# Kernel optimization log

Hardware: AMD Instinct MI355X
Metric: run time of the kernel (lower is better)

The kernel has to match this reference:

```python
import jax, jax.numpy as jnp
import numpy as np

HEADS = 16
DIM_HEAD = 64


def setup_inputs() -> dict:
    key = jax.random.key(0)
    k1, k2, k3 = jax.random.split(key, 3)
    b, n, dim = 4, 2048, 1024
    inner = HEADS * DIM_HEAD  # 1024
    x = jax.random.normal(k1, (b, n, dim), dtype=jnp.float32)
    # Dense weights, scaled like Glorot-ish init to keep softmax well-behaved
    w_qkv = jax.random.normal(k2, (dim, 3 * inner), dtype=jnp.float32) * (dim ** -0.5)
    w_out = jax.random.normal(k3, (inner, dim), dtype=jnp.float32) * (inner ** -0.5)
    b_out = jnp.zeros((dim,), dtype=jnp.float32)
    return {"x": x, "w_qkv": w_qkv, "w_out": w_out, "b_out": b_out}


def reference(x, w_qkv, w_out, b_out):
    b, n, dim = x.shape
    scale = DIM_HEAD ** -0.5
    qkv = x @ w_qkv  # [b, n, 3*h*d]
    q, k, v = jnp.split(qkv, 3, axis=-1)
    # 'b n (h d) -> b h n d'
    split_heads = lambda t: t.reshape(b, n, HEADS, DIM_HEAD).transpose(0, 2, 1, 3)
    q, k, v = split_heads(q), split_heads(k), split_heads(v)
    sim = jnp.einsum('bhid,bhjd->bhij', q, k) * scale  # [b, h, n, n]
    attn = jax.nn.softmax(sim, axis=-1)
    out = jnp.einsum('bhij,bhjd->bhid', attn, v)  # [b, h, n, d]
    out = out.transpose(0, 2, 1, 3).reshape(b, n, HEADS * DIM_HEAD)
    return out @ w_out + b_out  # dropout rate 0.0 -> identity
```

## Files before the change

### kernel.cpp

```cpp
#include <hip/hip_runtime.h>
#include <cstdint>

#define HEADS 16
#define DH 64
#define SEQ 2048
#define BATCH 4
#define DIM 1024
#define MTOT (BATCH*SEQ)
#define NQKV (3*DIM)

typedef short bf16x8 __attribute__((ext_vector_type(8)));
typedef float f32x4 __attribute__((ext_vector_type(4)));
typedef float f32x16 __attribute__((ext_vector_type(16)));

__device__ __forceinline__ unsigned short f2bf(float f) {
  union { float fv; unsigned int u; } c; c.fv = f;
  unsigned int u = c.u;
  u += 0x7FFFu + ((u >> 16) & 1u);
  return (unsigned short)(u >> 16);
}

__device__ __forceinline__ unsigned int pkbf(float lo, float hi) {
  union { float fv; unsigned int u; } a, b; a.fv = lo; b.fv = hi;
  return ((a.u + 0x8000u) >> 16) | ((b.u + 0x8000u) & 0xFFFF0000u);
}

__device__ __forceinline__ f32x4 mfma16(bf16x8 a, bf16x8 b, f32x4 c) {
  return __builtin_amdgcn_mfma_f32_16x16x32_bf16(a, b, c, 0, 0, 0);
}
__device__ __forceinline__ f32x16 mfma32(bf16x8 a, bf16x8 b, f32x16 c) {
  return __builtin_amdgcn_mfma_f32_32x32x16_bf16(a, b, c, 0, 0, 0);
}

typedef const __attribute__((address_space(1))) unsigned int* gas_ptr;
typedef __attribute__((address_space(3))) unsigned int* las_ptr;
__device__ __forceinline__ void gl2lds16(const void* g, void* l) {
  __builtin_amdgcn_global_load_lds((gas_ptr)g, (las_ptr)l, 16, 0, 0);
}

#define QSCALE 0.18033688011112042f

__global__ __launch_bounds__(256) void cast_f32_bf16(
    const float* __restrict__ in, unsigned short* __restrict__ out, int n4) {
  int i = blockIdx.x * blockDim.x + threadIdx.x;
  if (i >= n4) return;
  float4 v = reinterpret_cast<const float4*>(in)[i];
  uint2 o;
  o.x = (unsigned int)f2bf(v.x) | ((unsigned int)f2bf(v.y) << 16);
  o.y = (unsigned int)f2bf(v.z) | ((unsigned int)f2bf(v.w) << 16);
  reinterpret_cast<uint2*>(out)[i] = o;
}

__global__ __launch_bounds__(256) void transpose_cast(
    const float* __restrict__ in, unsigned short* __restrict__ out, int R, int C) {
  __shared__ float tile[32][33];
  int c0 = blockIdx.x * 32, r0 = blockIdx.y * 32;
  int tx = threadIdx.x & 31, ty = threadIdx.x >> 5;
  for (int i = 0; i < 32; i += 8)
    tile[ty + i][tx] = in[(size_t)(r0 + ty + i) * C + c0 + tx];
  __syncthreads();
  for (int i = 0; i < 32; i += 8)
    out[(size_t)(c0 + ty + i) * R + r0 + tx] = f2bf(tile[tx][ty + i]);
}

__global__ __launch_bounds__(256) void transpose_v(
    const unsigned short* __restrict__ V, unsigned short* __restrict__ Vt) {
  __shared__ unsigned short tile[64][72];
  int n0 = blockIdx.x * 64;
  size_t base = (size_t)blockIdx.y * SEQ * DH;
  int t = threadIdx.x;
  int r = t >> 2, c = (t & 3) * 8;
  *(uint4*)&tile[r][c]      = *(const uint4*)&V[base + (size_t)(n0 + r) * DH + c];
  *(uint4*)&tile[r][c + 32] = *(const uint4*)&V[base + (size_t)(n0 + r) * DH + c + 32];
  __syncthreads();
#pragma unroll
  for (int p = 0; p < 2; p++) {
    alignas(16) unsigned short tmp[8];
#pragma unroll
    for (int i = 0; i < 8; i++) tmp[i] = tile[c + p * 32 + i][r];
    *(uint4*)&Vt[base + (size_t)r * SEQ + n0 + c + p * 32] = *(uint4*)tmp;
  }
}

#define BM 128
#define BN 128
#define BK 32
#define LDT 32

__global__ __launch_bounds__(256) void gemm_qkv(
    const unsigned short* __restrict__ A, const unsigned short* __restrict__ Bt,
    unsigned short* __restrict__ Q, unsigned short* __restrict__ K,
    unsigned short* __restrict__ V) {
  __shared__ unsigned short sA[BM * LDT];
  __shared__ unsigned short sB[BN * LDT];
  const int KD = 1024;
  int m0 = blockIdx.y * BM;
  int n0 = blockIdx.x * BN;
  int t = threadIdx.x;
  int lane = t & 63, w = t >> 6;
  int wm = (w >> 1) * 64, wn = (w & 1) * 64;
  int fr = lane & 15, fq = (lane >> 4) * 8;

  const unsigned short* gA = &A[(size_t)(m0 + w * 16 + (lane >> 2)) * KD + (lane & 3) * 8];
  const unsigned short* gB = &Bt[(size_t)(n0 + w * 16 + (lane >> 2)) * KD + (lane & 3) * 8];
  char* lA = (char*)sA + w * 1024;
  char* lB = (char*)sB + w * 1024;

  f32x4 acc[4][4];
#pragma unroll
  for (int i = 0; i < 4; i++)
#pragma unroll
    for (int j = 0; j < 4; j++) { f32x4 z = {0.f, 0.f, 0.f, 0.f}; acc[i][j] = z; }

  for (int k0 = 0; k0 < KD; k0 += BK) {
    gl2lds16(gA + k0, lA);
    gl2lds16(gA + (size_t)64 * KD + k0, lA + 4096);
    gl2lds16(gB + k0, lB);
    gl2lds16(gB + (size_t)64 * KD + k0, lB + 4096);
    __syncthreads();
    bf16x8 af[4], bfr[4];
#pragma unroll
    for (int mt = 0; mt < 4; mt++)
      af[mt] = *reinterpret_cast<const bf16x8*>(&sA[(wm + mt * 16 + fr) * LDT + fq]);
#pragma unroll
    for (int nt = 0; nt < 4; nt++)
      bfr[nt] = *reinterpret_cast<const bf16x8*>(&sB[(wn + nt * 16 + fr) * LDT + fq]);
#pragma unroll
    for (int mt = 0; mt < 4; mt++)
#pragma unroll
      for (int nt = 0; nt < 4; nt++)
        acc[mt][nt] = mfma16(af[mt], bfr[nt], acc[mt][nt]);
    __syncthreads();
  }
  int rowq = (lane >> 4) * 4;
#pragma unroll
  for (int mt = 0; mt < 4; mt++)
#pragma unroll
    for (int nt = 0; nt < 4; nt++)
#pragma unroll
      for (int r = 0; r < 4; r++) {
        int m = m0 + wm + mt * 16 + rowq + r;
        int ncol = n0 + wn + nt * 16 + fr;
        int which = ncol >> 10;
        int hd = ncol & 1023;
        int b = m >> 11, nrow = m & 2047;
        float v = acc[mt][nt][r];
        if (which == 0) v *= QSCALE;
        unsigned short* dst = (which == 0) ? Q : (which == 1 ? K : V);
        size_t idx = ((size_t)(b * HEADS + (hd >> 6)) * SEQ + nrow) * DH + (hd & 63);
        dst[idx] = f2bf(v);
      }
}

__global__ __launch_bounds__(256) void gemm_out(
    const unsigned short* __restrict__ A, const unsigned short* __restrict__ Bt,
    const float* __restrict__ bias, float* __restrict__ C) {
  __shared__ unsigned short sA[BM * LDT];
  __shared__ unsigned short sB[BN * LDT];
  const int KD = 1024;
  int m0 = blockIdx.y * BM;
  int n0 = blockIdx.x * BN;
  int t = threadIdx.x;
  int lane = t & 63, w = t >> 6;
  int wm = (w >> 1) * 64, wn = (w & 1) * 64;
  int fr = lane & 15, fq = (lane >> 4) * 8;

  const unsigned short* gA = &A[(size_t)(m0 + w * 16 + (lane >> 2)) * KD + (lane & 3) * 8];
  const unsigned short* gB = &Bt[(size_t)(n0 + w * 16 + (lane >> 2)) * KD + (lane & 3) * 8];
  char* lA = (char*)sA + w * 1024;
  char* lB = (char*)sB + w * 1024;

  f32x4 acc[4][4];
#pragma unroll
  for (int i = 0; i < 4; i++)
#pragma unroll
    for (int j = 0; j < 4; j++) { f32x4 z = {0.f, 0.f, 0.f, 0.f}; acc[i][j] = z; }

  for (int k0 = 0; k0 < KD; k0 += BK) {
    gl2lds16(gA + k0, lA);
    gl2lds16(gA + (size_t)64 * KD + k0, lA + 4096);
    gl2lds16(gB + k0, lB);
    gl2lds16(gB + (size_t)64 * KD + k0, lB + 4096);
    __syncthreads();
    bf16x8 af[4], bfr[4];
#pragma unroll
    for (int mt = 0; mt < 4; mt++)
      af[mt] = *reinterpret_cast<const bf16x8*>(&sA[(wm + mt * 16 + fr) * LDT + fq]);
#pragma unroll
    for (int nt = 0; nt < 4; nt++)
      bfr[nt] = *reinterpret_cast<const bf16x8*>(&sB[(wn + nt * 16 + fr) * LDT + fq]);
#pragma unroll
    for (int mt = 0; mt < 4; mt++)
#pragma unroll
      for (int nt = 0; nt < 4; nt++)
        acc[mt][nt] = mfma16(af[mt], bfr[nt], acc[mt][nt]);
    __syncthreads();
  }
  int rowq = (lane >> 4) * 4;
#pragma unroll
  for (int mt = 0; mt < 4; mt++)
#pragma unroll
    for (int nt = 0; nt < 4; nt++)
#pragma unroll
      for (int r = 0; r < 4; r++) {
        int m = m0 + wm + mt * 16 + rowq + r;
        int ncol = n0 + wn + nt * 16 + fr;
        C[(size_t)m * DIM + ncol] = acc[mt][nt][r] + bias[ncol];
      }
}

#define LDA 72

__global__ __launch_bounds__(256, 2) void attention(
    const unsigned short* __restrict__ Qg, const unsigned short* __restrict__ Kg,
    const unsigned short* __restrict__ Vtg, unsigned short* __restrict__ Og) {
  __shared__ unsigned short smem[2 * 64 * LDA];
  unsigned short* sK  = smem;
  unsigned short* sVt = smem + 64 * LDA;
  int qb = blockIdx.x, h = blockIdx.y, b = blockIdx.z;
  size_t base = (size_t)(b * HEADS + h) * SEQ * DH;
  const unsigned short* Q = Qg + base;
  const unsigned short* K = Kg + base;
  const unsigned short* Vt = Vtg + base;
  int t = threadIdx.x, lane = t & 63, w = t >> 6;
  int m = lane & 31, kh = lane >> 5;
  int q0 = qb * 256 + w * 64;

  bf16x8 qf[2][4];
#pragma unroll
  for (int qh = 0; qh < 2; qh++)
#pragma unroll
    for (int kt = 0; kt < 4; kt++)
      qf[qh][kt] = *reinterpret_cast<const bf16x8*>(
          &Q[(size_t)(q0 + 32 * qh + m) * DH + kt * 16 + kh * 8]);

  f32x16 oaccT[2][2];
#pragma unroll
  for (int qh = 0; qh < 2; qh++)
#pragma unroll
    for (int dh = 0; dh < 2; dh++)
#pragma unroll
      for (int i = 0; i < 16; i++) oaccT[qh][dh][i] = 0.f;
  float rs[2] = {0.f, 0.f};

  int sr = t >> 2, sc = (t & 3) * 8;

  for (int j0 = 0; j0 < SEQ; j0 += 64) {
    *(uint4*)&sK[sr * LDA + sc]       = *(const uint4*)&K[(size_t)(j0 + sr) * DH + sc];
    *(uint4*)&sK[sr * LDA + sc + 32]  = *(const uint4*)&K[(size_t)(j0 + sr) * DH + sc + 32];
    *(uint4*)&sVt[sr * LDA + sc]      = *(const uint4*)&Vt[(size_t)sr * SEQ + j0 + sc];
    *(uint4*)&sVt[sr * LDA + sc + 32] = *(const uint4*)&Vt[(size_t)sr * SEQ + j0 + sc + 32];
    __syncthreads();

    unsigned int pp[2][8][2];
#pragma unroll
    for (int jt = 0; jt < 2; jt++) {
      bf16x8 kf[4];
#pragma unroll
      for (int kt = 0; kt < 4; kt++)
        kf[kt] = *reinterpret_cast<const bf16x8*>(
            &sK[(jt * 32 + m) * LDA + (2 * kt + kh) * 8]);
#pragma unroll
      for (int qh = 0; qh < 2; qh++) {
        f32x16 s;
#pragma unroll
        for (int i = 0; i < 16; i++) s[i] = 0.f;
#pragma unroll
        for (int kt = 0; kt < 4; kt++)
          s = mfma32(kf[kt], qf[qh][kt], s);
        float e[16];
#pragma unroll
        for (int i = 0; i < 16; i++) e[i] = __builtin_amdgcn_exp2f(s[i]);
        float t0 = (e[0] + e[1]) + (e[2] + e[3]);
        float t1 = (e[4] + e[5]) + (e[6] + e[7]);
        float t2 = (e[8] + e[9]) + (e[10] + e[11]);
        float t3 = (e[12] + e[13]) + (e[14] + e[15]);
        rs[qh] += (t0 + t1) + (t2 + t3);
#pragma unroll
        for (int sl = 0; sl < 4; sl++) {
          pp[qh][4 * jt + sl][0] = pkbf(e[4 * sl + 0], e[4 * sl + 1]);
          pp[qh][4 * jt + sl][1] = pkbf(e[4 * sl + 2], e[4 * sl + 3]);
        }
      }
    }

#pragma unroll
    for (int kb = 0; kb < 4; kb++) {
#pragma unroll
      for (int dh = 0; dh < 2; dh++) {
        union { uint2 u[2]; bf16x8 v; } ac;
        ac.u[0] = *(const uint2*)&sVt[(32 * dh + m) * LDA + 16 * kb + 4 * kh];
        ac.u[1] = *(const uint2*)&sVt[(32 * dh + m) * LDA + 16 * kb + 8 + 4 * kh];
#pragma unroll
        for (int qh = 0; qh < 2; qh++) {
          union { unsigned int u[4]; bf16x8 v; } bc;
          bc.u[0] = pp[qh][2 * kb][0];
          bc.u[1] = pp[qh][2 * kb][1];
          bc.u[2] = pp[qh][2 * kb + 1][0];
          bc.u[3] = pp[qh][2 * kb + 1][1];
          oaccT[qh][dh] = mfma32(ac.v, bc.v, oaccT[qh][dh]);
        }
      }
    }
    __syncthreads();
  }

  float inv[2];
#pragma unroll
  for (int qh = 0; qh < 2; qh++) {
    float tot = rs[qh] + __shfl_xor(rs[qh], 32);
    inv[qh] = 1.0f / tot;
  }

  unsigned int* ew = (unsigned int*)smem + (size_t)w * 32 * 36;
#pragma unroll
  for (int qh = 0; qh < 2; qh++) {
#pragma unroll
    for (int dh = 0; dh < 2; dh++)
#pragma unroll
      for (int sl = 0; sl < 4; sl++) {
        unsigned int u0 = pkbf(oaccT[qh][dh][4 * sl + 0] * inv[qh],
                               oaccT[qh][dh][4 * sl + 1] * inv[qh]);
        unsigned int u1 = pkbf(oaccT[qh][dh][4 * sl + 2] * inv[qh],
                               oaccT[qh][dh][4 * sl + 3] * inv[qh]);
        uint2 pk; pk.x = u0; pk.y = u1;
        *(uint2*)&ew[m * 36 + 16 * dh + 4 * sl + 2 * kh] = pk;
      }
    int mr = lane >> 3, ch = lane & 7;
#pragma unroll
    for (int it = 0; it < 4; it++) {
      uint4 vv = *(const uint4*)&ew[(8 * it + mr) * 36 + ch * 4];
      int n = q0 + 32 * qh + 8 * it + mr;
      *(uint4*)&Og[((size_t)(b * SEQ + n)) * DIM + h * DH + ch * 8] = vv;
    }
  }
}

extern "C" void kernel_launch(void* const* d_in, const int* in_sizes, int n_in,
                              void* d_out, int out_size, void* d_ws, size_t ws_size,
                              hipStream_t stream) {
  const float* x     = (const float*)d_in[0];
  const float* w_qkv = (const float*)d_in[1];
  const float* w_out = (const float*)d_in[2];
  const float* b_out = (const float*)d_in[3];
  float* out = (float*)d_out;

  char* ws = (char*)d_ws;
  unsigned short* xb     = (unsigned short*)ws; ws += (size_t)MTOT * DIM * 2;
  unsigned short* wqkv_t = (unsigned short*)ws; ws += (size_t)NQKV * DIM * 2;
  unsigned short* wout_t = (unsigned short*)ws; ws += (size_t)DIM * DIM * 2;
  unsigned short* qb_    = (unsigned short*)ws; ws += (size_t)BATCH * HEADS * SEQ * DH * 2;
  unsigned short* kb_    = (unsigned short*)ws; ws += (size_t)BATCH * HEADS * SEQ * DH * 2;
  unsigned short* vb_    = (unsigned short*)ws; ws += (size_t)BATCH * HEADS * SEQ * DH * 2;
  unsigned short* attnb  = (unsigned short*)ws; ws += (size_t)MTOT * DIM * 2;
  unsigned short* vt_    = xb;

  cast_f32_bf16<<<(MTOT * DIM / 4 + 255) / 256, 256, 0, stream>>>(x, xb, MTOT * DIM / 4);
  transpose_cast<<<dim3(NQKV / 32, DIM / 32), 256, 0, stream>>>(w_qkv, wqkv_t, DIM, NQKV);
  transpose_cast<<<dim3(DIM / 32, DIM / 32), 256, 0, stream>>>(w_out, wout_t, DIM, DIM);

  gemm_qkv<<<dim3(NQKV / BN, MTOT / BM), 256, 0, stream>>>(xb, wqkv_t, qb_, kb_, vb_);

  transpose_v<<<dim3(SEQ / 64, BATCH * HEADS), 256, 0, stream>>>(vb_, vt_);

  attention<<<dim3(SEQ / 256, HEADS, BATCH), 256, 0, stream>>>(qb_, kb_, vt_, attnb);

  gemm_out<<<dim3(DIM / BN, MTOT / BM), 256, 0, stream>>>(attnb, wout_t, b_out, out);
}
```

Before: 273.6 us.

## Shrink attention query tile, raise occupancy, swizzle block order, use hardware bf16 pack

Each attention block now covers 128 query rows instead of 256, so each wave owns 32 rows instead of 64. The kernel is launched with twice as many blocks and a launch bound of 4 blocks per CU, cutting register pressure so more waves can hide latency. Block indices are remapped so that consecutive blocks spread over different (batch, head) pairs, and the LDS row stride is changed from 72 to 68 with 8-byte stores and loads. Float-to-bf16 packing now uses the v_cvt_pk_bf16_f32 instruction in place of integer bit manipulation. In exchange, K/V tiles are loaded twice as often per query row, which doubles global and LDS traffic per unit of compute.

After: 269.5 us. About the same (-1.5%).

```diff
diff --git a/kernel.cpp b/kernel.cpp
--- a/kernel.cpp
+++ b/kernel.cpp
@@ -20,9 +20,10 @@
   return (unsigned short)(u >> 16);
 }
 
-__device__ __forceinline__ unsigned int pkbf(float lo, float hi) {
-  union { float fv; unsigned int u; } a, b; a.fv = lo; b.fv = hi;
-  return ((a.u + 0x8000u) >> 16) | ((b.u + 0x8000u) & 0xFFFF0000u);
+__device__ __forceinline__ unsigned int cvtpk(float lo, float hi) {
+  unsigned int r;
+  asm("v_cvt_pk_bf16_f32 %0, %1, %2" : "=v"(r) : "v"(lo), "v"(hi));
+  return r;
 }
 
 __device__ __forceinline__ f32x4 mfma16(bf16x8 a, bf16x8 b, f32x4 c) {
@@ -209,78 +210,94 @@
       }
 }
 
-#define LDA 72
-
-__global__ __launch_bounds__(256, 2) void attention(
+#define LDA 68
+
+__global__ __launch_bounds__(256, 4) void attention(
     const unsigned short* __restrict__ Qg, const unsigned short* __restrict__ Kg,
     const unsigned short* __restrict__ Vtg, unsigned short* __restrict__ Og) {
-  __shared__ unsigned short smem[2 * 64 * LDA];
+  __shared__ unsigned short smem[2 * 64 * 72];
   unsigned short* sK  = smem;
   unsigned short* sVt = smem + 64 * LDA;
-  int qb = blockIdx.x, h = blockIdx.y, b = blockIdx.z;
+
+  int gid = blockIdx.x + 16 * (blockIdx.y + 16 * blockIdx.z);
+  int qb   = (gid >> 3) & 15;
+  int pair = ((gid & 7) << 3) | (gid >> 7);
+  int h = pair & 15, b = pair >> 4;
+
   size_t base = (size_t)(b * HEADS + h) * SEQ * DH;
   const unsigned short* Q = Qg + base;
   const unsigned short* K = Kg + base;
   const unsigned short* Vt = Vtg + base;
   int t = threadIdx.x, lane = t & 63, w = t >> 6;
   int m = lane & 31, kh = lane >> 5;
-  int q0 = qb * 256 + w * 64;
-
-  bf16x8 qf[2][4];
-#pragma unroll
-  for (int qh = 0; qh < 2; qh++)
-#pragma unroll
-    for (int kt = 0; kt < 4; kt++)
-      qf[qh][kt] = *reinterpret_cast<const bf16x8*>(
-          &Q[(size_t)(q0 + 32 * qh + m) * DH + kt * 16 + kh * 8]);
-
-  f32x16 oaccT[2][2];
-#pragma unroll
-  for (int qh = 0; qh < 2; qh++)
-#pragma unroll
-    for (int dh = 0; dh < 2; dh++)
-#pragma unroll
-      for (int i = 0; i < 16; i++) oaccT[qh][dh][i] = 0.f;
-  float rs[2] = {0.f, 0.f};
+  int q0 = qb * 128 + w * 32;
+
+  bf16x8 qf[4];
+#pragma unroll
+  for (int kt = 0; kt < 4; kt++)
+    qf[kt] = *reinterpret_cast<const bf16x8*>(
+        &Q[(size_t)(q0 + m) * DH + kt * 16 + kh * 8]);
+
+  f32x16 oaccT[2];
+#pragma unroll
+  for (int dh = 0; dh < 2; dh++)
+#pragma unroll
+    for (int i = 0; i < 16; i++) oaccT[dh][i] = 0.f;
+  float rs = 0.f;
 
   int sr = t >> 2, sc = (t & 3) * 8;
 
   for (int j0 = 0; j0 < SEQ; j0 += 64) {
-    *(uint4*)&sK[sr * LDA + sc]       = *(const uint4*)&K[(size_t)(j0 + sr) * DH + sc];
-    *(uint4*)&sK[sr * LDA + sc + 32]  = *(const uint4*)&K[(size_t)(j0 + sr) * DH + sc + 32];
-    *(uint4*)&sVt[sr * LDA + sc]      = *(const uint4*)&Vt[(size_t)sr * SEQ + j0 + sc];
-    *(uint4*)&sVt[sr * LDA + sc + 32] = *(const uint4*)&Vt[(size_t)sr * SEQ + j0 + sc + 32];
-    __syncthreads();
-
-    unsigned int pp[2][8][2];
+    {
+      uint4 a0 = *(const uint4*)&K[(size_t)(j0 + sr) * DH + sc];
+      uint4 a1 = *(const uint4*)&K[(size_t)(j0 + sr) * DH + sc + 32];
+      uint4 b0 = *(const uint4*)&Vt[(size_t)sr * SEQ + j0 + sc];
+      uint4 b1 = *(const uint4*)&Vt[(size_t)sr * SEQ + j0 + sc + 32];
+      unsigned short* pk0 = &sK[sr * LDA + sc];
+      unsigned short* pk1 = &sK[sr * LDA + sc + 32];
+      unsigned short* pv0 = &sVt[sr * LDA + sc];
+      unsigned short* pv1 = &sVt[sr * LDA + sc + 32];
+      *(uint2*)pk0       = make_uint2(a0.x, a0.y);
+      *(uint2*)(pk0 + 4) = make_uint2(a0.z, a0.w);
+      *(uint2*)pk1       = make_uint2(a1.x, a1.y);
+      *(uint2*)(pk1 + 4) = make_uint2(a1.z, a1.w);
+      *(uint2*)pv0       = make_uint2(b0.x, b0.y);
+      *(uint2*)(pv0 + 4) = make_uint2(b0.z, b0.w);
+      *(uint2*)pv1       = make_uint2(b1.x, b1.y);
+      *(uint2*)(pv1 + 4) = make_uint2(b1.z, b1.w);
+    }
+    __syncthreads();
+
+    unsigned int pp[8][2];
 #pragma unroll
     for (int jt = 0; jt < 2; jt++) {
       bf16x8 kf[4];
 #pragma unroll
+      for (int kt = 0; kt < 4; kt++) {
+        union { uint2 u[2]; bf16x8 v; } kc;
+        const unsigned short* p = &sK[(jt * 32 + m) * LDA + (2 * kt + kh) * 8];
+        kc.u[0] = *(const uint2*)p;
+        kc.u[1] = *(const uint2*)(p + 4);
+        kf[kt] = kc.v;
+      }
+      f32x16 s;
+#pragma unroll
+      for (int i = 0; i < 16; i++) s[i] = 0.f;
+#pragma unroll
       for (int kt = 0; kt < 4; kt++)
-        kf[kt] = *reinterpret_cast<const bf16x8*>(
-            &sK[(jt * 32 + m) * LDA + (2 * kt + kh) * 8]);
-#pragma unroll
-      for (int qh = 0; qh < 2; qh++) {
-        f32x16 s;
-#pragma unroll
-        for (int i = 0; i < 16; i++) s[i] = 0.f;
-#pragma unroll
-        for (int kt = 0; kt < 4; kt++)
-          s = mfma32(kf[kt], qf[qh][kt], s);
-        float e[16];
-#pragma unroll
-        for (int i = 0; i < 16; i++) e[i] = __builtin_amdgcn_exp2f(s[i]);
-        float t0 = (e[0] + e[1]) + (e[2] + e[3]);
-        float t1 = (e[4] + e[5]) + (e[6] + e[7]);
-        float t2 = (e[8] + e[9]) + (e[10] + e[11]);
-        float t3 = (e[12] + e[13]) + (e[14] + e[15]);
-        rs[qh] += (t0 + t1) + (t2 + t3);
-#pragma unroll
-        for (int sl = 0; sl < 4; sl++) {
-          pp[qh][4 * jt + sl][0] = pkbf(e[4 * sl + 0], e[4 * sl + 1]);
-          pp[qh][4 * jt + sl][1] = pkbf(e[4 * sl + 2], e[4 * sl + 3]);
-        }
+        s = mfma32(kf[kt], qf[kt], s);
+      float e[16];
+#pragma unroll
+      for (int i = 0; i < 16; i++) e[i] = __builtin_amdgcn_exp2f(s[i]);
+      float t0 = (e[0] + e[1]) + (e[2] + e[3]);
+      float t1 = (e[4] + e[5]) + (e[6] + e[7]);
+      float t2 = (e[8] + e[9]) + (e[10] + e[11]);
+      float t3 = (e[12] + e[13]) + (e[14] + e[15]);
+      rs += (t0 + t1) + (t2 + t3);
+#pragma unroll
+      for (int sl = 0; sl < 4; sl++) {
+        pp[4 * jt + sl][0] = cvtpk(e[4 * sl + 0], e[4 * sl + 1]);
+        pp[4 * jt + sl][1] = cvtpk(e[4 * sl + 2], e[4 * sl + 3]);
       }
     }
 
@@ -289,48 +306,42 @@
 #pragma unroll
       for (int dh = 0; dh < 2; dh++) {
         union { uint2 u[2]; bf16x8 v; } ac;
-        ac.u[0] = *(const uint2*)&sVt[(32 * dh + m) * LDA + 16 * kb + 4 * kh];
-        ac.u[1] = *(const uint2*)&sVt[(32 * dh + m) * LDA + 16 * kb + 8 + 4 * kh];
-#pragma unroll
-        for (int qh = 0; qh < 2; qh++) {
-          union { unsigned int u[4]; bf16x8 v; } bc;
-          bc.u[0] = pp[qh][2 * kb][0];
-          bc.u[1] = pp[qh][2 * kb][1];
-          bc.u[2] = pp[qh][2 * kb + 1][0];
-          bc.u[3] = pp[qh][2 * kb + 1][1];
-          oaccT[qh][dh] = mfma32(ac.v, bc.v, oaccT[qh][dh]);
-        }
-      }
-    }
-    __syncthreads();
-  }
-
-  float inv[2];
-#pragma unroll
-  for (int qh = 0; qh < 2; qh++) {
-    float tot = rs[qh] + __shfl_xor(rs[qh], 32);
-    inv[qh] = 1.0f / tot;
+        const unsigned short* p = &sVt[(32 * dh + m) * LDA + 16 * kb + 4 * kh];
+        ac.u[0] = *(const uint2*)p;
+        ac.u[1] = *(const uint2*)(p + 8);
+        union { unsigned int u[4]; bf16x8 v; } bc;
+        bc.u[0] = pp[2 * kb][0];
+        bc.u[1] = pp[2 * kb][1];
+        bc.u[2] = pp[2 * kb + 1][0];
+        bc.u[3] = pp[2 * kb + 1][1];
+        oaccT[dh] = mfma32(ac.v, bc.v, oaccT[dh]);
+      }
+    }
+    __syncthreads();
+  }
+
+  float inv;
+  {
+    float tot = rs + __shfl_xor(rs, 32);
+    inv = 1.0f / tot;
   }
 
   unsigned int* ew = (unsigned int*)smem + (size_t)w * 32 * 36;
 #pragma unroll
-  for (int qh = 0; qh < 2; qh++) {
-#pragma unroll
-    for (int dh = 0; dh < 2; dh++)
-#pragma unroll
-      for (int sl = 0; sl < 4; sl++) {
-        unsigned int u0 = pkbf(oaccT[qh][dh][4 * sl + 0] * inv[qh],
-                               oaccT[qh][dh][4 * sl + 1] * inv[qh]);
-        unsigned int u1 = pkbf(oaccT[qh][dh][4 * sl + 2] * inv[qh],
-                               oaccT[qh][dh][4 * sl + 3] * inv[qh]);
-        uint2 pk; pk.x = u0; pk.y = u1;
-        *(uint2*)&ew[m * 36 + 16 * dh + 4 * sl + 2 * kh] = pk;
-      }
+  for (int dh = 0; dh < 2; dh++)
+#pragma unroll
+    for (int sl = 0; sl < 4; sl++) {
+      unsigned int u0 = cvtpk(oaccT[dh][4 * sl + 0] * inv, oaccT[dh][4 * sl + 1] * inv);
+      unsigned int u1 = cvtpk(oaccT[dh][4 * sl + 2] * inv, oaccT[dh][4 * sl + 3] * inv);
+      uint2 pk; pk.x = u0; pk.y = u1;
+      *(uint2*)&ew[m * 36 + 16 * dh + 4 * sl + 2 * kh] = pk;
+    }
+  {
     int mr = lane >> 3, ch = lane & 7;
 #pragma unroll
     for (int it = 0; it < 4; it++) {
       uint4 vv = *(const uint4*)&ew[(8 * it + mr) * 36 + ch * 4];
-      int n = q0 + 32 * qh + 8 * it + mr;
+      int n = q0 + 8 * it + mr;
       *(uint4*)&Og[((size_t)(b * SEQ + n)) * DIM + h * DH + ch * 8] = vv;
     }
   }
@@ -363,7 +374,7 @@
 
   transpose_v<<<dim3(SEQ / 64, BATCH * HEADS), 256, 0, stream>>>(vb_, vt_);
 
-  attention<<<dim3(SEQ / 256, HEADS, BATCH), 256, 0, stream>>>(qb_, kb_, vt_, attnb);
+  attention<<<dim3(SEQ / 128, HEADS, BATCH), 256, 0, stream>>>(qb_, kb_, vt_, attnb);
 
   gemm_out<<<dim3(DIM / BN, MTOT / BM), 256, 0, stream>>>(attnb, wout_t, b_out, out);
 }
```
